# Kernel tuning notes

Hardware: AMD Instinct MI355X
Metric: run time of the kernel (lower is better)

## Reference

```python
import jax, jax.numpy as jnp
import numpy as np

N, IN, H, C, E = 20000, 256, 256, 16, 640000

def sage_conv(x, edge_index, W_l, b_l, W_r):
    # PyG SAGEConv (aggr='mean', root_weight=True):
    # out = lin_l(mean_{j in N(i)} x_j) + lin_r(x_i)
    src, dst = edge_index[0], edge_index[1]
    n = x.shape[0]
    msgs = x[src]                                            # [E, d] irregular gather
    agg = jax.ops.segment_sum(msgs, dst, num_segments=n)     # [N, d]
    deg = jax.ops.segment_sum(jnp.ones((msgs.shape[0],), x.dtype), dst, num_segments=n)
    agg = agg / jnp.maximum(deg, 1.0)[:, None]               # mean aggregation
    return agg @ W_l + b_l + x @ W_r


def setup_inputs() -> dict:
    key = jax.random.key(0)
    ks = jax.random.split(key, 10)
    s = lambda k, fi, fo: jax.random.normal(k, (fi, fo), jnp.float32) / np.sqrt(fi)
    return {
        "x": jax.random.normal(ks[0], (N, IN), jnp.float32),
        "edge_index": jax.random.randint(ks[1], (2, E), 0, N, jnp.int64),
        "W1l": s(ks[2], IN, H), "b1": jnp.zeros((H,), jnp.float32), "W1r": s(ks[3], IN, H),
        "W2l": s(ks[4], H, H),  "b2": jnp.zeros((H,), jnp.float32), "W2r": s(ks[5], H, H),
        "Wc": s(ks[6], H, C),   "bc": jnp.zeros((C,), jnp.float32),
    }


def reference(x, edge_index, W1l, b1, W1r, W2l, b2, W2r, Wc, bc):
    h = sage_conv(x, edge_index, W1l, b1, W1r)
    h = jax.nn.relu(h)                    # dropout is identity in eval mode
    z = sage_conv(h, edge_index, W2l, b2, W2r)
    return z @ Wc + bc                    # classifier logits [N, C]
```

## Files before the change

kernel.cpp:

```cpp
#include <hip/hip_runtime.h>
#include <hip/hip_bf16.h>


#define FEAT 256
#define NCLS 16
#define ZPAD 264
#define MT   64
#define NSH  8
#define SCAP 64
#define SLOTS (NSH * SCAP)
#define CAPTOT 128

typedef __bf16 bf16x8 __attribute__((ext_vector_type(8)));
typedef __bf16 bf16x4 __attribute__((ext_vector_type(4)));
typedef float  f32x4  __attribute__((ext_vector_type(4)));
typedef float  f32x2  __attribute__((ext_vector_type(2)));
typedef unsigned int uint4v __attribute__((ext_vector_type(4)));

#define ACC8(S, U) do {                                                   \
    _Pragma("unroll")                                                     \
    for (int w_ = 0; w_ < 4; ++w_) {                                      \
        f32x2 lo_ = __builtin_amdgcn_cvt_pk_f32_fp8(U[w_], false);        \
        f32x2 hi_ = __builtin_amdgcn_cvt_pk_f32_fp8(U[w_], true);         \
        S[w_][0] += lo_[0]; S[w_][1] += lo_[1];                           \
        S[w_][2] += hi_[0]; S[w_][3] += hi_[1];                           \
    } } while (0)

__device__ __forceinline__ void load_entries(
    const int* __restrict__ cnt, const unsigned short* __restrict__ bucket,
    int node, int lane, int& e0, int& e1, int& deg, float& inv)
{
    int4 ca = *(const int4*)(cnt + node * NSH);
    int4 cb = *(const int4*)(cnt + node * NSH + 4);
    int cs[NSH] = {ca.x, ca.y, ca.z, ca.w, cb.x, cb.y, cb.z, cb.w};
    int ctrue = 0, d = 0;
    #pragma unroll
    for (int s = 0; s < NSH; ++s) {
        ctrue += cs[s];
        cs[s] = cs[s] < SCAP ? cs[s] : SCAP;
        d += cs[s];
    }
    deg = d < CAPTOT ? d : CAPTOT;
    inv = ctrue > 0 ? 1.0f / (float)ctrue : 0.0f;
    const unsigned short* lst = bucket + (size_t)node * SLOTS;

    auto get = [&](int i) -> int {
        int s = 0, loc = i;
        #pragma unroll
        for (int t = 0; t < NSH - 1; ++t) {
            if (s == t && loc >= cs[t]) { loc -= cs[t]; s = t + 1; }
        }
        return lst[s * SCAP + loc];
    };
    e0 = (lane < deg) ? get(lane) : 0;
    e1 = 0;
    if (deg > 64)
        e1 = (lane + 64 < deg) ? get(lane + 64) : 0;
}


__global__ __launch_bounds__(256) void fill_kernel(
    const int* __restrict__ src, const int* __restrict__ dst,
    int* __restrict__ cnt, unsigned short* __restrict__ bucket, int E)
{
    int sh = blockIdx.x & (NSH - 1);
    int e4 = (blockIdx.x * 256 + threadIdx.x) * 4;
    if (e4 + 3 < E) {
        int4 sv = *(const int4*)(src + e4);
        int4 dv = *(const int4*)(dst + e4);
        int p0 = atomicAdd(&cnt[dv.x * NSH + sh], 1);
        int p1 = atomicAdd(&cnt[dv.y * NSH + sh], 1);
        int p2 = atomicAdd(&cnt[dv.z * NSH + sh], 1);
        int p3 = atomicAdd(&cnt[dv.w * NSH + sh], 1);
        if (p0 < SCAP) bucket[(size_t)dv.x * SLOTS + sh * SCAP + p0] = (unsigned short)sv.x;
        if (p1 < SCAP) bucket[(size_t)dv.y * SLOTS + sh * SCAP + p1] = (unsigned short)sv.y;
        if (p2 < SCAP) bucket[(size_t)dv.z * SLOTS + sh * SCAP + p2] = (unsigned short)sv.z;
        if (p3 < SCAP) bucket[(size_t)dv.w * SLOTS + sh * SCAP + p3] = (unsigned short)sv.w;
    } else {
        for (int k = 0; k < 4 && e4 + k < E; ++k) {
            int s = src[e4 + k], d = dst[e4 + k];
            int p = atomicAdd(&cnt[d * NSH + sh], 1);
            if (p < SCAP) bucket[(size_t)d * SLOTS + sh * SCAP + p] = (unsigned short)s;
        }
    }
}


__global__ void cvt_kernel(const float* __restrict__ x,
                           const float* __restrict__ W1l, const float* __restrict__ W1r,
                           const float* __restrict__ W2l, const float* __restrict__ W2r,
                           const float* __restrict__ Wc, const float* __restrict__ b2,
                           const float* __restrict__ bc,
                           __bf16* __restrict__ xb, unsigned char* __restrict__ x8,
                           __bf16* __restrict__ W1lT, __bf16* __restrict__ W1rT,
                           __bf16* __restrict__ WaT, __bf16* __restrict__ WbT,
                           float* __restrict__ bc2,
                           int n4, int nb_cvt) {
    int t = threadIdx.x;
    int bx = blockIdx.x;
    if (bx < nb_cvt) {
        int i = bx * 256 + t;
        if (i < n4) {
            f32x4 v = ((const f32x4*)x)[i];
            bf16x4 o;
            #pragma unroll
            for (int j = 0; j < 4; ++j) o[j] = (__bf16)v[j];
            ((bf16x4*)xb)[i] = o;
            int pk = 0;
            pk = __builtin_amdgcn_cvt_pk_fp8_f32(v[0], v[1], pk, false);
            pk = __builtin_amdgcn_cvt_pk_fp8_f32(v[2], v[3], pk, true);
            ((int*)x8)[i] = pk;
        }
    } else if (bx < nb_cvt + 512) {
        int b = bx - nb_cvt;
        int w = b >> 8, nn = b & 255;
        const float* W = w ? W1r : W1l;
        __bf16* WT = w ? W1rT : W1lT;
        WT[nn * FEAT + t] = (__bf16)W[t * FEAT + nn];
    } else if (bx < nb_cvt + 512 + 32) {
        int b = bx - nb_cvt - 512;
        int c = b & 15;
        const float* W = (b < 16) ? W2l : W2r;
        __bf16* WT = (b < 16) ? WaT : WbT;
        float s = 0.f;
        #pragma unroll 4
        for (int m = 0; m < FEAT; ++m)
            s += W[t * FEAT + m] * Wc[m * NCLS + c];
        WT[c * FEAT + t] = (__bf16)s;
    } else {
        if (t < NCLS) {
            float s = 0.f;
            for (int k = 0; k < FEAT; ++k) s += b2[k] * Wc[k * NCLS + t];
            bc2[t] = s + bc[t];
        }
    }
}


__global__ __launch_bounds__(256) void agg_fp8_kernel(
    const unsigned char* __restrict__ t8, const int* __restrict__ cnt,
    const unsigned short* __restrict__ bucket, __bf16* __restrict__ out, int n)
{
    int wave = threadIdx.x >> 6;
    int node = blockIdx.x * 4 + wave;
    if (node >= n) return;
    int lane = threadIdx.x & 63;
    int quad = lane >> 4, l16 = lane & 15;

    int e0, e1, deg; float inv;
    load_entries(cnt, bucket, node, lane, e0, e1, deg, inv);

    f32x4 s0[4], s1[4];
    #pragma unroll
    for (int w = 0; w < 4; ++w) { s0[w] = (f32x4){0.f,0.f,0.f,0.f}; s1[w] = (f32x4){0.f,0.f,0.f,0.f}; }

    int nfull = deg >> 2;
    int rem   = deg & 3;
    const unsigned char* base = t8 + l16 * 16;

    int tt = 0;
    for (; tt + 7 < nfull; tt += 8) {
        int jj[8];
        #pragma unroll
        for (int u = 0; u < 8; ++u) {
            int i = (tt + u) * 4 + quad;
            jj[u] = (i < 64) ? __shfl(e0, i) : __shfl(e1, i - 64);
        }
        uint4v uu[8];
        #pragma unroll
        for (int u = 0; u < 8; ++u)
            uu[u] = *(const uint4v*)(base + (size_t)jj[u] * FEAT);
        #pragma unroll
        for (int u = 0; u < 8; ++u) {
            if (u & 1) ACC8(s1, uu[u]); else ACC8(s0, uu[u]);
        }
    }
    for (; tt + 3 < nfull; tt += 4) {
        int i0 = (tt + 0) * 4 + quad, i1 = (tt + 1) * 4 + quad;
        int i2 = (tt + 2) * 4 + quad, i3 = (tt + 3) * 4 + quad;
        int j0 = (i0 < 64) ? __shfl(e0, i0) : __shfl(e1, i0 - 64);
        int j1 = (i1 < 64) ? __shfl(e0, i1) : __shfl(e1, i1 - 64);
        int j2 = (i2 < 64) ? __shfl(e0, i2) : __shfl(e1, i2 - 64);
        int j3 = (i3 < 64) ? __shfl(e0, i3) : __shfl(e1, i3 - 64);
        uint4v u0 = *(const uint4v*)(base + (size_t)j0 * FEAT);
        uint4v u1 = *(const uint4v*)(base + (size_t)j1 * FEAT);
        uint4v u2 = *(const uint4v*)(base + (size_t)j2 * FEAT);
        uint4v u3 = *(const uint4v*)(base + (size_t)j3 * FEAT);
        ACC8(s0, u0); ACC8(s1, u1); ACC8(s0, u2); ACC8(s1, u3);
    }
    for (; tt < nfull; ++tt) {
        int i = tt * 4 + quad;
        int j = (i < 64) ? __shfl(e0, i) : __shfl(e1, i - 64);
        uint4v u = *(const uint4v*)(base + (size_t)j * FEAT);
        ACC8(s0, u);
    }
    if (rem) {
        int i = nfull * 4 + quad;
        int j = (i < 64) ? __shfl(e0, i) : __shfl(e1, i - 64);
        if (quad < rem) {
            uint4v u = *(const uint4v*)(base + (size_t)j * FEAT);
            ACC8(s1, u);
        }
    }

    #pragma unroll
    for (int w = 0; w < 4; ++w)
        #pragma unroll
        for (int j = 0; j < 4; ++j) {
            float v = s0[w][j] + s1[w][j];
            v += __shfl_xor(v, 16, 64);
            v += __shfl_xor(v, 32, 64);
            s0[w][j] = v;
        }

    bf16x4 o;
    #pragma unroll
    for (int j = 0; j < 4; ++j) o[j] = (__bf16)(s0[quad][j] * inv);
    *(bf16x4*)(out + (size_t)node * FEAT + l16 * 16 + quad * 4) = o;
}


__global__ __launch_bounds__(256) void gemm1_kernel(
    const __bf16* __restrict__ A1, const __bf16* __restrict__ A2,
    const __bf16* __restrict__ B1T, const __bf16* __restrict__ B2T,
    const float* __restrict__ bias,
    const __bf16* __restrict__ WaT, const __bf16* __restrict__ WbT,
    const float* __restrict__ bc2,
    __bf16* __restrict__ pb, float* __restrict__ q, int M)
{
    __shared__ __align__(16) __bf16 lds[2][MT][ZPAD];

    int m0   = blockIdx.x * MT;
    int t    = threadIdx.x;
    int lane = t & 63;
    int wave = t >> 6;
    int l16  = lane & 15, quad = lane >> 4;

    #pragma unroll 4
    for (int it = 0; it < 16; ++it) {
        int i = it * 256 + t;
        int pass = i >> 11;
        int r    = (i >> 5) & 63;
        int c8   = (i & 31) * 8;
        int gr = m0 + r; gr = (gr < M) ? gr : (M - 1);
        const __bf16* A = pass ? A2 : A1;
        *(bf16x8*)(&lds[pass][r][c8]) = *(const bf16x8*)(A + (size_t)gr * FEAT + c8);
    }
    __syncthreads();

    f32x4 acc[4][4];
    #pragma unroll
    for (int a = 0; a < 4; ++a)
        #pragma unroll
        for (int b = 0; b < 4; ++b) acc[a][b] = (f32x4){0.f, 0.f, 0.f, 0.f};

    int nbase = wave * 64;

    #pragma unroll 1
    for (int pass = 0; pass < 2; ++pass) {
        const __bf16* BT = pass ? B2T : B1T;
        #pragma unroll 2
        for (int kk = 0; kk < 8; ++kk) {
            int k0 = kk * 32 + quad * 8;
            bf16x8 af[4], bfm[4];
            #pragma unroll
            for (int mf = 0; mf < 4; ++mf)
                af[mf] = *(const bf16x8*)(&lds[pass][mf * 16 + l16][k0]);
            #pragma unroll
            for (int nt = 0; nt < 4; ++nt)
                bfm[nt] = *(const bf16x8*)(BT + (size_t)(nbase + nt * 16 + l16) * FEAT + k0);
            #pragma unroll
            for (int mf = 0; mf < 4; ++mf)
                #pragma unroll
                for (int nt = 0; nt < 4; ++nt)
                    acc[mf][nt] = __builtin_amdgcn_mfma_f32_16x16x32_bf16(
                        af[mf], bfm[nt], acc[mf][nt], 0, 0, 0);
        }
    }
    __syncthreads();

    #pragma unroll
    for (int nt = 0; nt < 4; ++nt) {
        int col = nbase + nt * 16 + l16;
        float bv = bias[col];
        #pragma unroll
        for (int mf = 0; mf < 4; ++mf) {
            int lr = mf * 16 + quad * 4;
            #pragma unroll
            for (int rr = 0; rr < 4; ++rr) {
                float v = acc[mf][nt][rr] + bv;
                lds[0][lr + rr][col] = (__bf16)(v > 0.f ? v : 0.f);
            }
        }
    }
    __syncthreads();

    {
        int half = wave >> 1;
        const __bf16* WT = (wave & 1) ? WbT : WaT;
        f32x4 a0 = (f32x4){0.f, 0.f, 0.f, 0.f};
        f32x4 a1 = (f32x4){0.f, 0.f, 0.f, 0.f};
        #pragma unroll 2
        for (int kk = 0; kk < 8; ++kk) {
            int k0 = kk * 32 + quad * 8;
            bf16x8 bv = *(const bf16x8*)(WT + (size_t)l16 * FEAT + k0);
            bf16x8 av0 = *(const bf16x8*)(&lds[0][half * 32 + l16][k0]);
            bf16x8 av1 = *(const bf16x8*)(&lds[0][half * 32 + 16 + l16][k0]);
            a0 = __builtin_amdgcn_mfma_f32_16x16x32_bf16(av0, bv, a0, 0, 0, 0);
            a1 = __builtin_amdgcn_mfma_f32_16x16x32_bf16(av1, bv, a1, 0, 0, 0);
        }
        #pragma unroll
        for (int mf = 0; mf < 2; ++mf) {
            f32x4 a = mf ? a1 : a0;
            if (wave & 1) {
                float qv = bc2[l16];
                #pragma unroll
                for (int rr = 0; rr < 4; ++rr) {
                    int row = m0 + half * 32 + mf * 16 + quad * 4 + rr;
                    if (row < M) q[(size_t)row * NCLS + l16] = a[rr] + qv;
                }
            } else {
                #pragma unroll
                for (int rr = 0; rr < 4; ++rr) {
                    int row = m0 + half * 32 + mf * 16 + quad * 4 + rr;
                    if (row < M) pb[(size_t)row * NCLS + l16] = (__bf16)a[rr];
                }
            }
        }
    }
}


__global__ __launch_bounds__(256) void agg_out_kernel(
    const __bf16* __restrict__ pb, const float* __restrict__ q,
    const int* __restrict__ cnt, const unsigned short* __restrict__ bucket,
    float* __restrict__ out, int n)
{
    int wave = threadIdx.x >> 6;
    int node = blockIdx.x * 4 + wave;
    if (node >= n) return;
    int lane = threadIdx.x & 63;
    int slot = lane >> 2, fq = lane & 3;

    int e0, e1, deg; float inv;
    load_entries(cnt, bucket, node, lane, e0, e1, deg, inv);

    f32x4 acc = {0.f, 0.f, 0.f, 0.f};
    for (int g = 0; g < deg; g += 32) {
        int i0 = g + slot, i1 = g + 16 + slot;
        int j0 = (i0 < 64) ? __shfl(e0, i0) : __shfl(e1, i0 - 64);
        int j1 = (i1 < 64) ? __shfl(e0, i1) : __shfl(e1, i1 - 64);
        bf16x4 a0 = *(const bf16x4*)(pb + (size_t)j0 * NCLS + fq * 4);
        bf16x4 a1 = *(const bf16x4*)(pb + (size_t)j1 * NCLS + fq * 4);
        float m0 = (i0 < deg) ? 1.f : 0.f;
        float m1 = (i1 < deg) ? 1.f : 0.f;
        #pragma unroll
        for (int k = 0; k < 4; ++k)
            acc[k] += m0 * (float)a0[k] + m1 * (float)a1[k];
    }

    #pragma unroll
    for (int k = 0; k < 4; ++k) {
        float v = acc[k];
        v += __shfl_xor(v, 4, 64);
        v += __shfl_xor(v, 8, 64);
        v += __shfl_xor(v, 16, 64);
        v += __shfl_xor(v, 32, 64);
        acc[k] = v;
    }

    if (slot == 0) {
        f32x4 qv = *(const f32x4*)(q + (size_t)node * NCLS + fq * 4);
        f32x4 o;
        #pragma unroll
        for (int k = 0; k < 4; ++k) o[k] = acc[k] * inv + qv[k];
        *(f32x4*)(out + (size_t)node * NCLS + fq * 4) = o;
    }
}


extern "C" void kernel_launch(void* const* d_in, const int* in_sizes, int n_in,
                              void* d_out, int out_size, void* d_ws, size_t ws_size,
                              hipStream_t stream) {
    const float* x   = (const float*)d_in[0];
    const int*   ei  = (const int*)d_in[1];
    const float* W1l = (const float*)d_in[2];
    const float* b1  = (const float*)d_in[3];
    const float* W1r = (const float*)d_in[4];
    const float* W2l = (const float*)d_in[5];
    const float* b2  = (const float*)d_in[6];
    const float* W2r = (const float*)d_in[7];
    const float* Wc  = (const float*)d_in[8];
    const float* bc  = (const float*)d_in[9];
    float* out = (float*)d_out;

    const int n = in_sizes[0] / FEAT;
    const int E = in_sizes[1] / 2;
    const int* srcp = ei;
    const int* dstp = ei + E;

    char* p = (char*)d_ws;
    auto alloc = [&](size_t bytes) { char* r = p; p += (bytes + 511) & ~511ull; return r; };
    int* cnt       = (int*)alloc((size_t)n * NSH * 4);
    unsigned short* bucket = (unsigned short*)alloc((size_t)n * SLOTS * 2);
    __bf16* W1lT   = (__bf16*)alloc((size_t)FEAT * FEAT * 2);
    __bf16* W1rT   = (__bf16*)alloc((size_t)FEAT * FEAT * 2);
    __bf16* WaT    = (__bf16*)alloc((size_t)NCLS * FEAT * 2);
    __bf16* WbT    = (__bf16*)alloc((size_t)NCLS * FEAT * 2);
    float*  bc2    = (float*)alloc((size_t)NCLS * 4);
    __bf16* xb     = (__bf16*)alloc((size_t)n * FEAT * 2);
    unsigned char* x8 = (unsigned char*)alloc((size_t)n * FEAT);
    __bf16* aggb   = (__bf16*)alloc((size_t)n * FEAT * 2);
    __bf16* pb     = (__bf16*)alloc((size_t)n * NCLS * 2);
    float*  qb     = (float*)alloc((size_t)n * NCLS * 4);

    int n4 = n * FEAT / 4;
    int nb_cvt  = (n4 + 255) / 256;
    int nb_fill = (E + 1023) / 1024;

    hipMemsetAsync(cnt, 0, (size_t)n * NSH * 4, stream);

    fill_kernel<<<nb_fill, 256, 0, stream>>>(srcp, dstp, cnt, bucket, E);

    cvt_kernel<<<nb_cvt + 512 + 32 + 1, 256, 0, stream>>>(
        x, W1l, W1r, W2l, W2r, Wc, b2, bc,
        xb, x8, W1lT, W1rT, WaT, WbT, bc2, n4, nb_cvt);

    agg_fp8_kernel<<<(n + 3) / 4, 256, 0, stream>>>(x8, cnt, bucket, aggb, n);
    gemm1_kernel<<<(n + MT - 1) / MT, 256, 0, stream>>>(aggb, xb, W1lT, W1rT, b1,
                                                        WaT, WbT, bc2, pb, qb, n);

    agg_out_kernel<<<(n + 3) / 4, 256, 0, stream>>>(pb, qb, cnt, bucket, out, n);
}
```

Before: 197.0 us.

## Merge edge bucketing into conversion kernel and branch-free masked gather loop

```diff
diff --git a/kernel.cpp b/kernel.cpp
--- a/kernel.cpp
+++ b/kernel.cpp
@@ -17,13 +17,13 @@
 typedef float  f32x2  __attribute__((ext_vector_type(2)));
 typedef unsigned int uint4v __attribute__((ext_vector_type(4)));
 
-#define ACC8(S, U) do {                                                   \
+#define ACCM(S, U, M) do {                                                \
     _Pragma("unroll")                                                     \
     for (int w_ = 0; w_ < 4; ++w_) {                                      \
         f32x2 lo_ = __builtin_amdgcn_cvt_pk_f32_fp8(U[w_], false);        \
         f32x2 hi_ = __builtin_amdgcn_cvt_pk_f32_fp8(U[w_], true);         \
-        S[w_][0] += lo_[0]; S[w_][1] += lo_[1];                           \
-        S[w_][2] += hi_[0]; S[w_][3] += hi_[1];                           \
+        S[w_][0] += M * lo_[0]; S[w_][1] += M * lo_[1];                   \
+        S[w_][2] += M * hi_[0]; S[w_][3] += M * hi_[1];                   \
     } } while (0)
 
 __device__ __forceinline__ void load_entries(
@@ -59,43 +59,18 @@
 }
 
 
-__global__ __launch_bounds__(256) void fill_kernel(
-    const int* __restrict__ src, const int* __restrict__ dst,
-    int* __restrict__ cnt, unsigned short* __restrict__ bucket, int E)
-{
-    int sh = blockIdx.x & (NSH - 1);
-    int e4 = (blockIdx.x * 256 + threadIdx.x) * 4;
-    if (e4 + 3 < E) {
-        int4 sv = *(const int4*)(src + e4);
-        int4 dv = *(const int4*)(dst + e4);
-        int p0 = atomicAdd(&cnt[dv.x * NSH + sh], 1);
-        int p1 = atomicAdd(&cnt[dv.y * NSH + sh], 1);
-        int p2 = atomicAdd(&cnt[dv.z * NSH + sh], 1);
-        int p3 = atomicAdd(&cnt[dv.w * NSH + sh], 1);
-        if (p0 < SCAP) bucket[(size_t)dv.x * SLOTS + sh * SCAP + p0] = (unsigned short)sv.x;
-        if (p1 < SCAP) bucket[(size_t)dv.y * SLOTS + sh * SCAP + p1] = (unsigned short)sv.y;
-        if (p2 < SCAP) bucket[(size_t)dv.z * SLOTS + sh * SCAP + p2] = (unsigned short)sv.z;
-        if (p3 < SCAP) bucket[(size_t)dv.w * SLOTS + sh * SCAP + p3] = (unsigned short)sv.w;
-    } else {
-        for (int k = 0; k < 4 && e4 + k < E; ++k) {
-            int s = src[e4 + k], d = dst[e4 + k];
-            int p = atomicAdd(&cnt[d * NSH + sh], 1);
-            if (p < SCAP) bucket[(size_t)d * SLOTS + sh * SCAP + p] = (unsigned short)s;
-        }
-    }
-}
-
-
-__global__ void cvt_kernel(const float* __restrict__ x,
-                           const float* __restrict__ W1l, const float* __restrict__ W1r,
-                           const float* __restrict__ W2l, const float* __restrict__ W2r,
-                           const float* __restrict__ Wc, const float* __restrict__ b2,
-                           const float* __restrict__ bc,
-                           __bf16* __restrict__ xb, unsigned char* __restrict__ x8,
-                           __bf16* __restrict__ W1lT, __bf16* __restrict__ W1rT,
-                           __bf16* __restrict__ WaT, __bf16* __restrict__ WbT,
-                           float* __restrict__ bc2,
-                           int n4, int nb_cvt) {
+__global__ void combo_kernel(const float* __restrict__ x,
+                             const float* __restrict__ W1l, const float* __restrict__ W1r,
+                             const float* __restrict__ W2l, const float* __restrict__ W2r,
+                             const float* __restrict__ Wc, const float* __restrict__ b2,
+                             const float* __restrict__ bc,
+                             const int* __restrict__ src, const int* __restrict__ dst,
+                             __bf16* __restrict__ xb, unsigned char* __restrict__ x8,
+                             __bf16* __restrict__ W1lT, __bf16* __restrict__ W1rT,
+                             __bf16* __restrict__ WaT, __bf16* __restrict__ WbT,
+                             float* __restrict__ bc2,
+                             int* __restrict__ cnt, unsigned short* __restrict__ bucket,
+                             int n4, int E, int nb_cvt) {
     int t = threadIdx.x;
     int bx = blockIdx.x;
     if (bx < nb_cvt) {
@@ -127,11 +102,25 @@
         for (int m = 0; m < FEAT; ++m)
             s += W[t * FEAT + m] * Wc[m * NCLS + c];
         WT[c * FEAT + t] = (__bf16)s;
-    } else {
+    } else if (bx == nb_cvt + 512 + 32) {
         if (t < NCLS) {
             float s = 0.f;
             for (int k = 0; k < FEAT; ++k) s += b2[k] * Wc[k * NCLS + t];
             bc2[t] = s + bc[t];
+        }
+    } else {
+        int sh = bx & (NSH - 1);
+        int idx = (bx - nb_cvt - 512 - 33) * 256 + t;
+        int e2 = idx * 2;
+        if (e2 < E) {
+            int2 sv = *(const int2*)(src + e2);
+            int2 dv = *(const int2*)(dst + e2);
+            int p0 = atomicAdd(&cnt[dv.x * NSH + sh], 1);
+            if (p0 < SCAP) bucket[(size_t)dv.x * SLOTS + sh * SCAP + p0] = (unsigned short)sv.x;
+            if (e2 + 1 < E) {
+                int p1 = atomicAdd(&cnt[dv.y * NSH + sh], 1);
+                if (p1 < SCAP) bucket[(size_t)dv.y * SLOTS + sh * SCAP + p1] = (unsigned short)sv.y;
+            }
         }
     }
 }
@@ -154,52 +143,41 @@
     #pragma unroll
     for (int w = 0; w < 4; ++w) { s0[w] = (f32x4){0.f,0.f,0.f,0.f}; s1[w] = (f32x4){0.f,0.f,0.f,0.f}; }
 
-    int nfull = deg >> 2;
-    int rem   = deg & 3;
+    int rounds = (deg + 3) >> 2;
     const unsigned char* base = t8 + l16 * 16;
 
-    int tt = 0;
-    for (; tt + 7 < nfull; tt += 8) {
-        int jj[8];
+    {
+        int jj[8]; float mm[8];
         #pragma unroll
         for (int u = 0; u < 8; ++u) {
+            int i = u * 4 + quad;
+            jj[u] = __shfl(e0, i);
+            mm[u] = (i < deg) ? 1.f : 0.f;
+        }
+        uint4v uu[8];
+        #pragma unroll
+        for (int u = 0; u < 8; ++u)
+            uu[u] = *(const uint4v*)(base + (size_t)jj[u] * FEAT);
+        #pragma unroll
+        for (int u = 0; u < 8; ++u) {
+            if (u & 1) ACCM(s1, uu[u], mm[u]); else ACCM(s0, uu[u], mm[u]);
+        }
+    }
+    for (int tt = 8; tt < rounds; tt += 4) {
+        int jj[4]; float mm[4];
+        #pragma unroll
+        for (int u = 0; u < 4; ++u) {
             int i = (tt + u) * 4 + quad;
             jj[u] = (i < 64) ? __shfl(e0, i) : __shfl(e1, i - 64);
-        }
-        uint4v uu[8];
-        #pragma unroll
-        for (int u = 0; u < 8; ++u)
+            mm[u] = (i < deg) ? 1.f : 0.f;
+        }
+        uint4v uu[4];
+        #pragma unroll
+        for (int u = 0; u < 4; ++u)
             uu[u] = *(const uint4v*)(base + (size_t)jj[u] * FEAT);
         #pragma unroll
-        for (int u = 0; u < 8; ++u) {
-            if (u & 1) ACC8(s1, uu[u]); else ACC8(s0, uu[u]);
-        }
-    }
-    for (; tt + 3 < nfull; tt += 4) {
-        int i0 = (tt + 0) * 4 + quad, i1 = (tt + 1) * 4 + quad;
-        int i2 = (tt + 2) * 4 + quad, i3 = (tt + 3) * 4 + quad;
-        int j0 = (i0 < 64) ? __shfl(e0, i0) : __shfl(e1, i0 - 64);
-        int j1 = (i1 < 64) ? __shfl(e0, i1) : __shfl(e1, i1 - 64);
-        int j2 = (i2 < 64) ? __shfl(e0, i2) : __shfl(e1, i2 - 64);
-        int j3 = (i3 < 64) ? __shfl(e0, i3) : __shfl(e1, i3 - 64);
-        uint4v u0 = *(const uint4v*)(base + (size_t)j0 * FEAT);
-        uint4v u1 = *(const uint4v*)(base + (size_t)j1 * FEAT);
-        uint4v u2 = *(const uint4v*)(base + (size_t)j2 * FEAT);
-        uint4v u3 = *(const uint4v*)(base + (size_t)j3 * FEAT);
-        ACC8(s0, u0); ACC8(s1, u1); ACC8(s0, u2); ACC8(s1, u3);
-    }
-    for (; tt < nfull; ++tt) {
-        int i = tt * 4 + quad;
-        int j = (i < 64) ? __shfl(e0, i) : __shfl(e1, i - 64);
-        uint4v u = *(const uint4v*)(base + (size_t)j * FEAT);
-        ACC8(s0, u);
-    }
-    if (rem) {
-        int i = nfull * 4 + quad;
-        int j = (i < 64) ? __shfl(e0, i) : __shfl(e1, i - 64);
-        if (quad < rem) {
-            uint4v u = *(const uint4v*)(base + (size_t)j * FEAT);
-            ACC8(s1, u);
+        for (int u = 0; u < 4; ++u) {
+            if (u & 1) ACCM(s1, uu[u], mm[u]); else ACCM(s0, uu[u], mm[u]);
         }
     }
 
@@ -416,15 +394,13 @@
 
     int n4 = n * FEAT / 4;
     int nb_cvt  = (n4 + 255) / 256;
-    int nb_fill = (E + 1023) / 1024;
+    int nb_edge = (E + 511) / 512;
 
     hipMemsetAsync(cnt, 0, (size_t)n * NSH * 4, stream);
 
-    fill_kernel<<<nb_fill, 256, 0, stream>>>(srcp, dstp, cnt, bucket, E);
-
-    cvt_kernel<<<nb_cvt + 512 + 32 + 1, 256, 0, stream>>>(
-        x, W1l, W1r, W2l, W2r, Wc, b2, bc,
-        xb, x8, W1lT, W1rT, WaT, WbT, bc2, n4, nb_cvt);
+    combo_kernel<<<nb_cvt + 512 + 32 + 1 + nb_edge, 256, 0, stream>>>(
+        x, W1l, W1r, W2l, W2r, Wc, b2, bc, srcp, dstp,
+        xb, x8, W1lT, W1rT, WaT, WbT, bc2, cnt, bucket, n4, E, nb_cvt);
 
     agg_fp8_kernel<<<(n + 3) / 4, 256, 0, stream>>>(x8, cnt, bucket, aggb, n);
     gemm1_kernel<<<(n + MT - 1) / MT, 256, 0, stream>>>(aggb, xb, W1lT, W1rT, b1,
```

Result: faster. 182.3 us (-7.5%).
